# Kernel tuning notes

Measured on AMD Instinct MI355X. Metric: run time of the kernel, lower is better.

## Reference

```python
import jax, jax.numpy as jnp
import numpy as np

NHEAD = 8
DIM_HEAD = 64
SCALE = DIM_HEAD ** (-0.5)


def setup_inputs() -> dict:
    key = jax.random.key(0)
    k1, k2, k3 = jax.random.split(key, 3)
    B, C, X, Y = 16, 256, 64, 64
    x = jax.random.normal(k1, (B, C, X, Y), dtype=jnp.float32)
    # 1x1 conv weights, represented as [out_channels, in_channels]
    w_qkv = jax.random.normal(k2, (3 * NHEAD * DIM_HEAD, C), dtype=jnp.float32) * (C ** -0.5)
    w_out = jax.random.normal(k3, (C, NHEAD * DIM_HEAD), dtype=jnp.float32) * ((NHEAD * DIM_HEAD) ** -0.5)
    return {"x": x, "w_qkv": w_qkv, "w_out": w_out}


def reference(x, w_qkv, w_out):
    B, C, X, Y = x.shape
    h, d = NHEAD, DIM_HEAD
    n = X * Y
    # 1x1 conv == channel-wise matmul
    qkv = jnp.einsum('bcxy,oc->boxy', x, w_qkv)          # [B, 3*h*d, X, Y]
    qkv = qkv.reshape(B, 3, h, d, n)                     # chunk along channels then (h c)
    q, k, v = qkv[:, 0], qkv[:, 1], qkv[:, 2]            # each [B, h, d, n]
    q = jax.nn.softmax(q, axis=-2) * SCALE               # softmax over feature dim d
    k = jax.nn.softmax(k, axis=-1)                       # softmax over token dim n
    phi_kv = jnp.einsum('bhdn,bhen->bhde', k, v)         # [B, h, d, d]
    att = jnp.einsum('bhde,bhdn->bhen', phi_kv, q)       # [B, h, d, n]
    att = att.reshape(B, h * d, X, Y)
    out = jnp.einsum('bexy,ce->bcxy', att, w_out)        # [B, C, X, Y]
    return out
```

## Files before the change

### kernel.cpp

```cpp
#include <hip/hip_runtime.h>
#include <hip/hip_bf16.h>


typedef __attribute__((ext_vector_type(8))) short bf16x8;
typedef __attribute__((ext_vector_type(4))) float f32x4;

__device__ __forceinline__ unsigned short f2bf(float f) {
    union { float f; unsigned int i; } w; w.f = f;
    unsigned int r = w.i + 0x7FFFu + ((w.i >> 16) & 1u);
    return (unsigned short)(r >> 16);
}

__global__ __launch_bounds__(256) void cvt_w_frag(
    const float* __restrict__ wqkv, unsigned short* __restrict__ wf)
{
    int g = blockIdx.x * 256 + threadIdx.x;
    int lane = g & 63;
    int ks   = (g >> 6) & 7;
    int w2   = (g >> 9) & 3;
    int h    = (g >> 11) & 7;
    int op   = g >> 14;
    int row = op * 512 + h * 64 + w2 * 16 + (lane & 15);
    int col = ks * 32 + (lane >> 4) * 8;
    const float* src = &wqkv[(size_t)row * 256 + col];
    float4 f0 = *(const float4*)&src[0];
    float4 f1 = *(const float4*)&src[4];
    unsigned short t[8] = {f2bf(f0.x), f2bf(f0.y), f2bf(f0.z), f2bf(f0.w),
                           f2bf(f1.x), f2bf(f1.y), f2bf(f1.z), f2bf(f1.w)};
    *(uint4*)&wf[(size_t)g * 8] = *(uint4*)t;
}

__global__ __launch_bounds__(256) void cvt_xT(
    const float* __restrict__ x, unsigned short* __restrict__ xT)
{
    const int nb = blockIdx.x * 64, cb = blockIdx.y * 64, b = blockIdx.z;
    __shared__ float Ts[64 * 65];
    const int tid = threadIdx.x;
    const int l = tid & 63, w = tid >> 6;
    const float* xb = x + ((size_t)b * 256 + cb) * 4096 + nb;
#pragma unroll
    for (int p = 0; p < 4; p++) {
        int c = p * 16 + (tid >> 4);
        int n4 = (tid & 15) * 4;
        float4 v = *(const float4*)&xb[(size_t)c * 4096 + n4];
        Ts[c * 65 + n4 + 0] = v.x; Ts[c * 65 + n4 + 1] = v.y;
        Ts[c * 65 + n4 + 2] = v.z; Ts[c * 65 + n4 + 3] = v.w;
    }
    __syncthreads();
    unsigned short t[16];
#pragma unroll
    for (int i = 0; i < 16; i++) t[i] = f2bf(Ts[(w * 16 + i) * 65 + l]);
    unsigned short* dst = xT + ((size_t)b * 4096 + nb + l) * 256 + cb + w * 16;
    *(uint4*)&dst[0] = *(uint4*)&t[0];
    *(uint4*)&dst[8] = *(uint4*)&t[8];
}

__global__ __launch_bounds__(256, 3) void q_gemm(
    const unsigned short* __restrict__ xT, const unsigned short* __restrict__ wf,
    unsigned short* __restrict__ qf)
{
    const int ch = blockIdx.x;
    const int h  = blockIdx.y;
    const int b  = blockIdx.z;
    const int tid  = threadIdx.x;
    const int lane = tid & 63;
    const int w    = tid >> 6;
    const int quad = lane >> 4;
    const int l15  = lane & 15;

    __shared__ unsigned short smem[18432];
    unsigned short* Bs = smem;
    float* red = (float*)smem;
    unsigned short* Qs = smem + 9216;

    const unsigned short* wfq = wf + ((size_t)((0 * 8 + h) * 4 + w) * 8) * 512 + lane * 8;

    const int srow = tid >> 1;
    const int sch  = (tid & 1) * 32;

    for (int st = 0; st < 4; st++) {
        const int nb = ch * 512 + st * 128;
        const unsigned short* xrow =
            xT + ((size_t)b * 4096 + nb + srow) * 256 + sch;

        f32x4 accq[8];
#pragma unroll
        for (int i = 0; i < 8; i++) accq[i] = (f32x4)(0.f);

        {
            uint4 p0 = *(const uint4*)&xrow[0];
            uint4 p1 = *(const uint4*)&xrow[8];
            uint4 p2 = *(const uint4*)&xrow[16];
            uint4 p3 = *(const uint4*)&xrow[24];
            unsigned short* bw = Bs + srow * 72 + sch;
            *(uint4*)&bw[0]  = p0; *(uint4*)&bw[8]  = p1;
            *(uint4*)&bw[16] = p2; *(uint4*)&bw[24] = p3;
        }
        __syncthreads();

        for (int ks = 0; ks < 4; ks++) {
            const int buf = ks & 1;
            uint4 n0, n1, n2, n3;
            if (ks < 3) {
                n0 = *(const uint4*)&xrow[(ks + 1) * 64];
                n1 = *(const uint4*)&xrow[(ks + 1) * 64 + 8];
                n2 = *(const uint4*)&xrow[(ks + 1) * 64 + 16];
                n3 = *(const uint4*)&xrow[(ks + 1) * 64 + 24];
            }
            bf16x8 aq0 = *(const bf16x8*)&wfq[(2 * ks) * 512];
            bf16x8 aq1 = *(const bf16x8*)&wfq[(2 * ks + 1) * 512];
            const unsigned short* bsr = Bs + buf * 9216 + l15 * 72 + quad * 8;
#pragma unroll
            for (int nt = 0; nt < 8; nt++) {
                bf16x8 bv0 = *(const bf16x8*)&bsr[nt * 1152];
                bf16x8 bv1 = *(const bf16x8*)&bsr[nt * 1152 + 32];
                accq[nt] = __builtin_amdgcn_mfma_f32_16x16x32_bf16(aq0, bv0, accq[nt], 0, 0, 0);
                accq[nt] = __builtin_amdgcn_mfma_f32_16x16x32_bf16(aq1, bv1, accq[nt], 0, 0, 0);
            }
            if (ks < 3) {
                unsigned short* bw = Bs + (buf ^ 1) * 9216 + srow * 72 + sch;
                *(uint4*)&bw[0]  = n0; *(uint4*)&bw[8]  = n1;
                *(uint4*)&bw[16] = n2; *(uint4*)&bw[24] = n3;
                __syncthreads();
            }
        }

#pragma unroll
        for (int nt = 0; nt < 8; nt++) {
#pragma unroll
            for (int r = 0; r < 4; r++) accq[nt][r] = __expf(accq[nt][r]);
            float s = accq[nt][0] + accq[nt][1] + accq[nt][2] + accq[nt][3];
            s += __shfl_xor(s, 16);
            s += __shfl_xor(s, 32);
            if (quad == 0) red[w * 128 + nt * 16 + l15] = s;
        }
        __syncthreads();
        if (tid < 128) {
            float t = red[tid] + red[128 + tid] + red[256 + tid] + red[384 + tid];
            red[512 + tid] = 0.125f / t;
        }
        __syncthreads();
#pragma unroll
        for (int nt = 0; nt < 8; nt++) {
            float li = red[512 + nt * 16 + l15];
            uint2 pp;
            pp.x = (unsigned int)f2bf(accq[nt][0] * li) |
                   ((unsigned int)f2bf(accq[nt][1] * li) << 16);
            pp.y = (unsigned int)f2bf(accq[nt][2] * li) |
                   ((unsigned int)f2bf(accq[nt][3] * li) << 16);
            *(uint2*)&Qs[(nt * 16 + l15) * 72 + w * 16 + quad * 4] = pp;
        }
        __syncthreads();
        {
            const int n = tid >> 1, half = tid & 1;
            const int nbIdx = ch * 4 + st;
            const int ksq = h * 2 + half;
            const size_t gbase =
                (((size_t)(b * 32 + nbIdx) * 16 + ksq) * 8 + (n >> 4)) * 64 + (n & 15);
#pragma unroll
            for (int u = 0; u < 4; u++)
                *(uint4*)&qf[(gbase + u * 16) * 8] = *(uint4*)&Qs[n * 72 + half * 32 + u * 8];
        }
    }
}

__global__ __launch_bounds__(256, 2) void kv_phi(
    const unsigned short* __restrict__ xT, const unsigned short* __restrict__ wf,
    float* __restrict__ phi, float* __restrict__ lsum)
{
    const int ch = blockIdx.x;
    const int h  = blockIdx.y;
    const int b  = blockIdx.z;
    const int tid  = threadIdx.x;
    const int lane = tid & 63;
    const int w    = tid >> 6;
    const int quad = lane >> 4;
    const int l15  = lane & 15;

    __shared__ unsigned short smem[18432];
    unsigned short* Es = smem;
    unsigned short* Vs = smem + 8192;
    unsigned short* Bs = smem;

    const unsigned short* wfk = wf + ((size_t)((1 * 8 + h) * 4 + w) * 8) * 512 + lane * 8;
    const unsigned short* wfv = wf + ((size_t)((2 * 8 + h) * 4 + w) * 8) * 512 + lane * 8;

    f32x4 pacc[4];
#pragma unroll
    for (int i = 0; i < 4; i++) pacc[i] = (f32x4)(0.f);
    float lacc[4] = {0.f, 0.f, 0.f, 0.f};

    const int srow = tid >> 1;
    const int sch  = (tid & 1) * 32;

    for (int st = 0; st < 4; st++) {
        const int nb = ch * 512 + st * 128;
        const unsigned short* xrow =
            xT + ((size_t)b * 4096 + nb + srow) * 256 + sch;

        f32x4 acck[8], accv[8];
#pragma unroll
        for (int i = 0; i < 8; i++) {
            acck[i] = (f32x4)(0.f); accv[i] = (f32x4)(0.f);
        }

        __syncthreads();
        {
            uint4 p0 = *(const uint4*)&xrow[0];
            uint4 p1 = *(const uint4*)&xrow[8];
            uint4 p2 = *(const uint4*)&xrow[16];
            uint4 p3 = *(const uint4*)&xrow[24];
            unsigned short* bw = Bs + srow * 72 + sch;
            *(uint4*)&bw[0]  = p0; *(uint4*)&bw[8]  = p1;
            *(uint4*)&bw[16] = p2; *(uint4*)&bw[24] = p3;
        }
        __syncthreads();

        for (int ks = 0; ks < 4; ks++) {
            const int buf = ks & 1;
            uint4 n0, n1, n2, n3;
            if (ks < 3) {
                n0 = *(const uint4*)&xrow[(ks + 1) * 64];
                n1 = *(const uint4*)&xrow[(ks + 1) * 64 + 8];
                n2 = *(const uint4*)&xrow[(ks + 1) * 64 + 16];
                n3 = *(const uint4*)&xrow[(ks + 1) * 64 + 24];
            }
            bf16x8 ak0 = *(const bf16x8*)&wfk[(2 * ks) * 512];
            bf16x8 ak1 = *(const bf16x8*)&wfk[(2 * ks + 1) * 512];
            bf16x8 av0 = *(const bf16x8*)&wfv[(2 * ks) * 512];
            bf16x8 av1 = *(const bf16x8*)&wfv[(2 * ks + 1) * 512];
            const unsigned short* bsr = Bs + buf * 9216 + l15 * 72 + quad * 8;
#pragma unroll
            for (int nt = 0; nt < 8; nt++) {
                bf16x8 bv0 = *(const bf16x8*)&bsr[nt * 1152];
                bf16x8 bv1 = *(const bf16x8*)&bsr[nt * 1152 + 32];
                acck[nt] = __builtin_amdgcn_mfma_f32_16x16x32_bf16(ak0, bv0, acck[nt], 0, 0, 0);
                accv[nt] = __builtin_amdgcn_mfma_f32_16x16x32_bf16(av0, bv0, accv[nt], 0, 0, 0);
                acck[nt] = __builtin_amdgcn_mfma_f32_16x16x32_bf16(ak1, bv1, acck[nt], 0, 0, 0);
                accv[nt] = __builtin_amdgcn_mfma_f32_16x16x32_bf16(av1, bv1, accv[nt], 0, 0, 0);
            }
            if (ks < 3) {
                unsigned short* bw = Bs + (buf ^ 1) * 9216 + srow * 72 + sch;
                *(uint4*)&bw[0]  = n0; *(uint4*)&bw[8]  = n1;
                *(uint4*)&bw[16] = n2; *(uint4*)&bw[24] = n3;
                __syncthreads();
            }
        }
        __syncthreads();

#pragma unroll
        for (int r = 0; r < 4; r++) {
            const int dl = quad * 4 + r;
            const int dbase = (w * 16 + dl) * 256 + (l15 & 7) * 2;
#pragma unroll
            for (int nt = 0; nt < 8; nt++) {
                const int pos = (2 * nt + (l15 >> 3)) ^ dl;
                float ek = __expf(acck[nt][r]);
                lacc[r] += ek;
                *(unsigned short*)((char*)Es + dbase + pos * 16) = f2bf(ek);
                *(unsigned short*)((char*)Vs + dbase + pos * 16) = f2bf(accv[nt][r]);
            }
        }
        __syncthreads();

#pragma unroll
        for (int k2 = 0; k2 < 4; k2++) {
            bf16x8 ae = *(bf16x8*)((char*)Es + (w * 16 + l15) * 256 +
                                   (((k2 * 4 + quad) ^ l15) * 16));
#pragma unroll
            for (int et = 0; et < 4; et++) {
                bf16x8 bv = *(bf16x8*)((char*)Vs + (et * 16 + l15) * 256 +
                                       (((k2 * 4 + quad) ^ l15) * 16));
                pacc[et] = __builtin_amdgcn_mfma_f32_16x16x32_bf16(ae, bv, pacc[et], 0, 0, 0);
            }
        }
    }

#pragma unroll
    for (int r = 0; r < 4; r++) {
        float s = lacc[r];
        s += __shfl_xor(s, 1); s += __shfl_xor(s, 2);
        s += __shfl_xor(s, 4); s += __shfl_xor(s, 8);
        if (l15 == 0)
            atomicAdd(&lsum[((size_t)b * 8 + h) * 64 + w * 16 + quad * 4 + r], s);
    }
    float* pp = phi + ((size_t)b * 8 + h) * 4096;
#pragma unroll
    for (int et = 0; et < 4; et++)
#pragma unroll
        for (int r = 0; r < 4; r++)
            atomicAdd(&pp[(w * 16 + quad * 4 + r) * 64 + et * 16 + l15], pacc[et][r]);
}

__global__ __launch_bounds__(256) void build_M(
    const float* __restrict__ phi, const float* __restrict__ lsum,
    const float* __restrict__ w_out, unsigned short* __restrict__ Mf)
{
    const int h = blockIdx.x, b = blockIdx.y;
    __shared__ float pT[64][68];
    const float* pp = phi + ((size_t)b * 8 + h) * 4096;
    const int tid = threadIdx.x;
    const int row = tid >> 2, ls = tid & 3;
#pragma unroll
    for (int u = 0; u < 4; u++) {
        int e0 = (ls + u * 4) * 4;
        float4 v = *(const float4*)&pp[row * 64 + e0];
        pT[e0 + 0][row] = v.x; pT[e0 + 1][row] = v.y;
        pT[e0 + 2][row] = v.z; pT[e0 + 3][row] = v.w;
    }
    __syncthreads();
    const int c = tid;
    float acc[64];
#pragma unroll
    for (int d = 0; d < 64; d++) acc[d] = 0.f;
    for (int e4 = 0; e4 < 16; e4++) {
        float4 wv = *(const float4*)&w_out[(size_t)c * 512 + h * 64 + e4 * 4];
        float wq[4] = {wv.x, wv.y, wv.z, wv.w};
#pragma unroll
        for (int qq = 0; qq < 4; qq++) {
            int e = e4 * 4 + qq;
#pragma unroll
            for (int d4 = 0; d4 < 16; d4++) {
                float4 p = *(const float4*)&pT[e][d4 * 4];
                acc[d4 * 4 + 0] += wq[qq] * p.x;
                acc[d4 * 4 + 1] += wq[qq] * p.y;
                acc[d4 * 4 + 2] += wq[qq] * p.z;
                acc[d4 * 4 + 3] += wq[qq] * p.w;
            }
        }
    }
    const float* lrow = lsum + ((size_t)b * 8 + h) * 64;
    unsigned short tmp[64];
#pragma unroll
    for (int d = 0; d < 64; d++) tmp[d] = f2bf(acc[d] / lrow[d]);
    const int ct = c >> 7, wr = (c >> 6) & 1, mi = (c >> 4) & 3, l15c = c & 15;
#pragma unroll
    for (int u = 0; u < 8; u++) {
        const int ksA = h * 2 + (u >> 2);
        const int quadA = u & 3;
        size_t gidx = ((((size_t)(b * 2 + ct) * 2 + wr) * 4 + mi) * 16 + ksA) * 64
                      + quadA * 16 + l15c;
        *(uint4*)&Mf[gidx * 8] = *(uint4*)&tmp[u * 8];
    }
}

__global__ __launch_bounds__(256, 3) void out_mfma(
    const unsigned short* __restrict__ Mf, const unsigned short* __restrict__ qf,
    float* __restrict__ out)
{
    const int nbIdx = blockIdx.x;
    const int ct    = blockIdx.y;
    const int b     = blockIdx.z;
    const int tid  = threadIdx.x;
    const int lane = tid & 63;
    const int w    = tid >> 6;
    const int wr   = w >> 1, wc = w & 1;
    const int quad = lane >> 4;
    const int l15  = lane & 15;

    f32x4 acc[4][4];
#pragma unroll
    for (int i = 0; i < 4; i++)
#pragma unroll
        for (int j = 0; j < 4; j++) acc[i][j] = (f32x4)(0.f);

    const unsigned short* Ab =
        Mf + ((((size_t)(b * 2 + ct) * 2 + wr) * 4) * 16) * 512 + lane * 8;
    const unsigned short* Bb =
        qf + (((size_t)(b * 32 + nbIdx) * 16) * 8) * 512 + lane * 8;

    for (int ks = 0; ks < 16; ks++) {
        bf16x8 af[4], bv[4];
#pragma unroll
        for (int mi = 0; mi < 4; mi++)
            af[mi] = *(const bf16x8*)&Ab[(size_t)(mi * 16 + ks) * 512];
#pragma unroll
        for (int ni = 0; ni < 4; ni++)
            bv[ni] = *(const bf16x8*)&Bb[(size_t)(ks * 8 + wc * 4 + ni) * 512];
#pragma unroll
        for (int mi = 0; mi < 4; mi++)
#pragma unroll
            for (int ni = 0; ni < 4; ni++)
                acc[mi][ni] = __builtin_amdgcn_mfma_f32_16x16x32_bf16(
                    af[mi], bv[ni], acc[mi][ni], 0, 0, 0);
    }
    float* ob = out + ((size_t)b * 256 + ct * 128 + wr * 64) * 4096
                + nbIdx * 128 + wc * 64;
#pragma unroll
    for (int mi = 0; mi < 4; mi++)
#pragma unroll
        for (int ni = 0; ni < 4; ni++)
#pragma unroll
            for (int r = 0; r < 4; r++)
                ob[(size_t)(mi * 16 + quad * 4 + r) * 4096 + ni * 16 + l15]
                    = acc[mi][ni][r];
}

extern "C" void kernel_launch(void* const* d_in, const int* in_sizes, int n_in,
                              void* d_out, int out_size, void* d_ws, size_t ws_size,
                              hipStream_t stream) {
    const float* x     = (const float*)d_in[0];
    const float* w_qkv = (const float*)d_in[1];
    const float* w_out = (const float*)d_in[2];
    float* out = (float*)d_out;

    char* ws = (char*)d_ws;
    unsigned short* qf = (unsigned short*)ws;
    unsigned short* wf = (unsigned short*)(ws + 67108864);
    float* lsum = (float*)(ws + 67895296);
    float* phi  = (float*)(ws + 67928064);
    unsigned short* Mf = (unsigned short*)(ws + 70025216);
    unsigned short* xT = (unsigned short*)(ws + 74219520);

    hipMemsetAsync(lsum, 0, (8192 + 524288) * sizeof(float), stream);

    cvt_w_frag<<<192, 256, 0, stream>>>(w_qkv, wf);
    cvt_xT<<<dim3(64, 4, 16), 256, 0, stream>>>(x, xT);
    q_gemm<<<dim3(8, 8, 16), 256, 0, stream>>>(xT, wf, qf);
    kv_phi<<<dim3(8, 8, 16), 256, 0, stream>>>(xT, wf, phi, lsum);
    build_M<<<dim3(8, 16), 256, 0, stream>>>(phi, lsum, w_out, Mf);
    out_mfma<<<dim3(32, 2, 16), 256, 0, stream>>>(Mf, qf, out);
}
```

Measured before the change: 277.5 us.

## Stage X tiles with direct global-to-LDS loads and XOR-swizzled layout

Replaces the register-staged copy of the activation tiles (global load into VGPRs, then an LDS store) with global_load_lds DMA-style 16-byte loads in both q_gemm and kv_phi. The LDS layout changes from padded rows to XOR-swizzled rows so the MFMA operand reads avoid bank conflicts without padding, which also shrinks shared memory. q_gemm additionally preloads all eight weight fragments into registers once instead of reloading them per k-step, and adds a barrier at the end of each stage. The aim is to cut VGPR pressure and instruction overhead on the load path and to overlap prefetch with MFMA. The risk is that the double-buffer synchronisation relies on barriers waiting for the async LDS writes to complete, and whether the compiler inserts the required vmcnt waits.

```diff
diff --git a/kernel.cpp b/kernel.cpp
--- a/kernel.cpp
+++ b/kernel.cpp
@@ -9,6 +9,13 @@
     union { float f; unsigned int i; } w; w.f = f;
     unsigned int r = w.i + 0x7FFFu + ((w.i >> 16) & 1u);
     return (unsigned short)(r >> 16);
+}
+
+__device__ __forceinline__ void gload16(const unsigned short* g, unsigned short* l) {
+    __builtin_amdgcn_global_load_lds(
+        (const __attribute__((address_space(1))) void*)(const void*)g,
+        (__attribute__((address_space(3))) void*)(void*)l,
+        16, 0, 0);
 }
 
 __global__ __launch_bounds__(256) void cvt_w_frag(
@@ -68,61 +75,54 @@
     const int quad = lane >> 4;
     const int l15  = lane & 15;
 
-    __shared__ unsigned short smem[18432];
+    __shared__ unsigned short smem[16384];
     unsigned short* Bs = smem;
     float* red = (float*)smem;
-    unsigned short* Qs = smem + 9216;
+    unsigned short* Qs = smem + 7168;
 
     const unsigned short* wfq = wf + ((size_t)((0 * 8 + h) * 4 + w) * 8) * 512 + lane * 8;
-
-    const int srow = tid >> 1;
-    const int sch  = (tid & 1) * 32;
+    bf16x8 aq[8];
+#pragma unroll
+    for (int i = 0; i < 8; i++) aq[i] = *(const bf16x8*)&wfq[i * 512];
+
+    const int grow = lane >> 3;
+    const int gch  = ((lane & 7) ^ grow) * 8;
+    const int c0 = (quad ^ (l15 & 7)) * 8;
+    const int c1 = ((quad + 4) ^ (l15 & 7)) * 8;
 
     for (int st = 0; st < 4; st++) {
         const int nb = ch * 512 + st * 128;
-        const unsigned short* xrow =
-            xT + ((size_t)b * 4096 + nb + srow) * 256 + sch;
+        const unsigned short* gbase =
+            xT + ((size_t)b * 4096 + nb + w * 32 + grow) * 256 + gch;
 
         f32x4 accq[8];
 #pragma unroll
         for (int i = 0; i < 8; i++) accq[i] = (f32x4)(0.f);
 
-        {
-            uint4 p0 = *(const uint4*)&xrow[0];
-            uint4 p1 = *(const uint4*)&xrow[8];
-            uint4 p2 = *(const uint4*)&xrow[16];
-            uint4 p3 = *(const uint4*)&xrow[24];
-            unsigned short* bw = Bs + srow * 72 + sch;
-            *(uint4*)&bw[0]  = p0; *(uint4*)&bw[8]  = p1;
-            *(uint4*)&bw[16] = p2; *(uint4*)&bw[24] = p3;
-        }
-        __syncthreads();
-
+#pragma unroll
+        for (int i = 0; i < 4; i++)
+            gload16(gbase + i * 2048, Bs + w * 2048 + i * 512);
+        __syncthreads();
+
+#pragma unroll
         for (int ks = 0; ks < 4; ks++) {
             const int buf = ks & 1;
-            uint4 n0, n1, n2, n3;
             if (ks < 3) {
-                n0 = *(const uint4*)&xrow[(ks + 1) * 64];
-                n1 = *(const uint4*)&xrow[(ks + 1) * 64 + 8];
-                n2 = *(const uint4*)&xrow[(ks + 1) * 64 + 16];
-                n3 = *(const uint4*)&xrow[(ks + 1) * 64 + 24];
-            }
-            bf16x8 aq0 = *(const bf16x8*)&wfq[(2 * ks) * 512];
-            bf16x8 aq1 = *(const bf16x8*)&wfq[(2 * ks + 1) * 512];
-            const unsigned short* bsr = Bs + buf * 9216 + l15 * 72 + quad * 8;
+                const unsigned short* gs = gbase + (ks + 1) * 64;
+                unsigned short* ld = Bs + (buf ^ 1) * 8192 + w * 2048;
+#pragma unroll
+                for (int i = 0; i < 4; i++)
+                    gload16(gs + i * 2048, ld + i * 512);
+            }
+            const unsigned short* bsr = Bs + buf * 8192 + l15 * 64;
 #pragma unroll
             for (int nt = 0; nt < 8; nt++) {
-                bf16x8 bv0 = *(const bf16x8*)&bsr[nt * 1152];
-                bf16x8 bv1 = *(const bf16x8*)&bsr[nt * 1152 + 32];
-                accq[nt] = __builtin_amdgcn_mfma_f32_16x16x32_bf16(aq0, bv0, accq[nt], 0, 0, 0);
-                accq[nt] = __builtin_amdgcn_mfma_f32_16x16x32_bf16(aq1, bv1, accq[nt], 0, 0, 0);
-            }
-            if (ks < 3) {
-                unsigned short* bw = Bs + (buf ^ 1) * 9216 + srow * 72 + sch;
-                *(uint4*)&bw[0]  = n0; *(uint4*)&bw[8]  = n1;
-                *(uint4*)&bw[16] = n2; *(uint4*)&bw[24] = n3;
-                __syncthreads();
-            }
+                bf16x8 bv0 = *(const bf16x8*)&bsr[nt * 1024 + c0];
+                bf16x8 bv1 = *(const bf16x8*)&bsr[nt * 1024 + c1];
+                accq[nt] = __builtin_amdgcn_mfma_f32_16x16x32_bf16(aq[2 * ks], bv0, accq[nt], 0, 0, 0);
+                accq[nt] = __builtin_amdgcn_mfma_f32_16x16x32_bf16(aq[2 * ks + 1], bv1, accq[nt], 0, 0, 0);
+            }
+            if (ks < 3) __syncthreads();
         }
 
 #pragma unroll
@@ -155,12 +155,13 @@
             const int n = tid >> 1, half = tid & 1;
             const int nbIdx = ch * 4 + st;
             const int ksq = h * 2 + half;
-            const size_t gbase =
+            const size_t gbase2 =
                 (((size_t)(b * 32 + nbIdx) * 16 + ksq) * 8 + (n >> 4)) * 64 + (n & 15);
 #pragma unroll
             for (int u = 0; u < 4; u++)
-                *(uint4*)&qf[(gbase + u * 16) * 8] = *(uint4*)&Qs[n * 72 + half * 32 + u * 8];
-        }
+                *(uint4*)&qf[(gbase2 + u * 16) * 8] = *(uint4*)&Qs[n * 72 + half * 32 + u * 8];
+        }
+        __syncthreads();
     }
 }
 
@@ -177,7 +178,7 @@
     const int quad = lane >> 4;
     const int l15  = lane & 15;
 
-    __shared__ unsigned short smem[18432];
+    __shared__ unsigned short smem[16384];
     unsigned short* Es = smem;
     unsigned short* Vs = smem + 8192;
     unsigned short* Bs = smem;
@@ -190,13 +191,15 @@
     for (int i = 0; i < 4; i++) pacc[i] = (f32x4)(0.f);
     float lacc[4] = {0.f, 0.f, 0.f, 0.f};
 
-    const int srow = tid >> 1;
-    const int sch  = (tid & 1) * 32;
+    const int grow = lane >> 3;
+    const int gch  = ((lane & 7) ^ grow) * 8;
+    const int c0 = (quad ^ (l15 & 7)) * 8;
+    const int c1 = ((quad + 4) ^ (l15 & 7)) * 8;
 
     for (int st = 0; st < 4; st++) {
         const int nb = ch * 512 + st * 128;
-        const unsigned short* xrow =
-            xT + ((size_t)b * 4096 + nb + srow) * 256 + sch;
+        const unsigned short* gbase =
+            xT + ((size_t)b * 4096 + nb + w * 32 + grow) * 256 + gch;
 
         f32x4 acck[8], accv[8];
 #pragma unroll
@@ -205,46 +208,36 @@
         }
 
         __syncthreads();
-        {
-            uint4 p0 = *(const uint4*)&xrow[0];
-            uint4 p1 = *(const uint4*)&xrow[8];
-            uint4 p2 = *(const uint4*)&xrow[16];
-            uint4 p3 = *(const uint4*)&xrow[24];
-            unsigned short* bw = Bs + srow * 72 + sch;
-            *(uint4*)&bw[0]  = p0; *(uint4*)&bw[8]  = p1;
-            *(uint4*)&bw[16] = p2; *(uint4*)&bw[24] = p3;
-        }
-        __syncthreads();
-
+#pragma unroll
+        for (int i = 0; i < 4; i++)
+            gload16(gbase + i * 2048, Bs + w * 2048 + i * 512);
+        __syncthreads();
+
+#pragma unroll
         for (int ks = 0; ks < 4; ks++) {
             const int buf = ks & 1;
-            uint4 n0, n1, n2, n3;
             if (ks < 3) {
-                n0 = *(const uint4*)&xrow[(ks + 1) * 64];
-                n1 = *(const uint4*)&xrow[(ks + 1) * 64 + 8];
-                n2 = *(const uint4*)&xrow[(ks + 1) * 64 + 16];
-                n3 = *(const uint4*)&xrow[(ks + 1) * 64 + 24];
+                const unsigned short* gs = gbase + (ks + 1) * 64;
+                unsigned short* ld = Bs + (buf ^ 1) * 8192 + w * 2048;
+#pragma unroll
+                for (int i = 0; i < 4; i++)
+                    gload16(gs + i * 2048, ld + i * 512);
             }
             bf16x8 ak0 = *(const bf16x8*)&wfk[(2 * ks) * 512];
             bf16x8 ak1 = *(const bf16x8*)&wfk[(2 * ks + 1) * 512];
             bf16x8 av0 = *(const bf16x8*)&wfv[(2 * ks) * 512];
             bf16x8 av1 = *(const bf16x8*)&wfv[(2 * ks + 1) * 512];
-            const unsigned short* bsr = Bs + buf * 9216 + l15 * 72 + quad * 8;
+            const unsigned short* bsr = Bs + buf * 8192 + l15 * 64;
 #pragma unroll
             for (int nt = 0; nt < 8; nt++) {
-                bf16x8 bv0 = *(const bf16x8*)&bsr[nt * 1152];
-                bf16x8 bv1 = *(const bf16x8*)&bsr[nt * 1152 + 32];
+                bf16x8 bv0 = *(const bf16x8*)&bsr[nt * 1024 + c0];
+                bf16x8 bv1 = *(const bf16x8*)&bsr[nt * 1024 + c1];
                 acck[nt] = __builtin_amdgcn_mfma_f32_16x16x32_bf16(ak0, bv0, acck[nt], 0, 0, 0);
                 accv[nt] = __builtin_amdgcn_mfma_f32_16x16x32_bf16(av0, bv0, accv[nt], 0, 0, 0);
                 acck[nt] = __builtin_amdgcn_mfma_f32_16x16x32_bf16(ak1, bv1, acck[nt], 0, 0, 0);
                 accv[nt] = __builtin_amdgcn_mfma_f32_16x16x32_bf16(av1, bv1, accv[nt], 0, 0, 0);
             }
-            if (ks < 3) {
-                unsigned short* bw = Bs + (buf ^ 1) * 9216 + srow * 72 + sch;
-                *(uint4*)&bw[0]  = n0; *(uint4*)&bw[8]  = n1;
-                *(uint4*)&bw[16] = n2; *(uint4*)&bw[24] = n3;
-                __syncthreads();
-            }
+            if (ks < 3) __syncthreads();
         }
         __syncthreads();
 
```

Result: faster. 262.9 us (-5.3%).
